# Kernel tuning notes

Measured on AMD Instinct MI355X. Metric: run time of the kernel, lower is better.

## Reference

```python
import jax, jax.numpy as jnp
import numpy as np

VOCAB = 32000
EMBED = 128
HIDDEN = 2048
LAYERS = 3
BATCH = 16


def setup_inputs() -> dict:
    key = jax.random.key(0)
    ks = jax.random.split(key, 4 + 4 * LAYERS)
    inp = {}
    inp["tokens"] = jax.random.randint(ks[0], (1, BATCH), 0, VOCAB, dtype=jnp.int64)
    inp["hidden"] = jax.random.normal(ks[1], (LAYERS, BATCH, HIDDEN), dtype=jnp.float32)
    s_e = 1.0 / np.sqrt(EMBED)
    s_h = 1.0 / np.sqrt(HIDDEN)
    inp["emb"] = jax.random.normal(ks[2], (VOCAB, EMBED), dtype=jnp.float32) * s_e
    for l in range(LAYERS):
        in_dim = EMBED if l == 0 else HIDDEN
        k0, k1, k2, k3 = jax.random.split(ks[4 + l], 4)
        inp[f"W_ih{l}"] = jax.random.normal(k0, (3 * HIDDEN, in_dim), dtype=jnp.float32) * s_h
        inp[f"W_hh{l}"] = jax.random.normal(k1, (3 * HIDDEN, HIDDEN), dtype=jnp.float32) * s_h
        inp[f"b_ih{l}"] = jax.random.normal(k2, (3 * HIDDEN,), dtype=jnp.float32) * s_h
        inp[f"b_hh{l}"] = jax.random.normal(k3, (3 * HIDDEN,), dtype=jnp.float32) * s_h
    inp["W_out"] = jax.random.normal(ks[3], (VOCAB, HIDDEN), dtype=jnp.float32) * s_h
    inp["b_out"] = jnp.zeros((VOCAB,), dtype=jnp.float32)
    return inp


def _gru_cell(x, h, W_ih, W_hh, b_ih, b_hh):
    # PyTorch GRU gate math; x: (B, in), h: (B, H)
    gi = x @ W_ih.T + b_ih  # (B, 3H)
    gh = h @ W_hh.T + b_hh  # (B, 3H)
    i_r, i_z, i_n = jnp.split(gi, 3, axis=-1)
    h_r, h_z, h_n = jnp.split(gh, 3, axis=-1)
    r = jax.nn.sigmoid(i_r + h_r)
    z = jax.nn.sigmoid(i_z + h_z)
    n = jnp.tanh(i_n + r * h_n)
    return (1.0 - z) * n + z * h


def reference(tokens, hidden, emb,
              W_ih0, W_hh0, b_ih0, b_hh0,
              W_ih1, W_hh1, b_ih1, b_hh1,
              W_ih2, W_hh2, b_ih2, b_hh2,
              W_out, b_out):
    # embedding + ReLU; tokens: (1, B) -> x: (B, E) (seq_len = 1)
    x = jax.nn.relu(emb[tokens[0]])
    Ws = [(W_ih0, W_hh0, b_ih0, b_hh0),
          (W_ih1, W_hh1, b_ih1, b_hh1),
          (W_ih2, W_hh2, b_ih2, b_hh2)]
    new_h = []
    inp = x
    for l, (Wih, Whh, bih, bhh) in enumerate(Ws):
        h_l = _gru_cell(inp, hidden[l], Wih, Whh, bih, bhh)
        new_h.append(h_l)
        inp = h_l  # top-layer output feeds next layer
    new_hidden = jnp.stack(new_h, axis=0)  # (L, B, H)
    logits = inp @ W_out.T + b_out  # (B, V)
    logp = jax.nn.log_softmax(logits, axis=1)
    return logp, new_hidden
```

## Files before the change

kernel.cpp:

```cpp
#include <hip/hip_runtime.h>
#include <cmath>


#define BB 16
#define HH 2048
#define EE 128
#define VV 32000
#define G3H (3 * HH)

__device__ __forceinline__ void fma4(float& a, const float4 w, const float4 x) {
  a = fmaf(w.x, x.x, a); a = fmaf(w.y, x.y, a);
  a = fmaf(w.z, x.z, a); a = fmaf(w.w, x.w, a);
}

__device__ __forceinline__ void glds16(const float* g, float* l) {
  __builtin_amdgcn_global_load_lds(
      (__attribute__((address_space(1))) void*)(g),
      (__attribute__((address_space(3))) void*)(l), 16, 0, 0);
}

__device__ __forceinline__ float foldpair(float a, float b, int m, int lane) {
  float t = (lane & m) ? a : b;
  t = __shfl_xor(t, m, 64);
  return ((lane & m) ? b : a) + t;
}

__device__ __forceinline__ float sel16(const float a[16], int i) {
  float s0 = (i & 1) ? a[1]  : a[0];
  float s1 = (i & 1) ? a[3]  : a[2];
  float s2 = (i & 1) ? a[5]  : a[4];
  float s3 = (i & 1) ? a[7]  : a[6];
  float s4 = (i & 1) ? a[9]  : a[8];
  float s5 = (i & 1) ? a[11] : a[10];
  float s6 = (i & 1) ? a[13] : a[12];
  float s7 = (i & 1) ? a[15] : a[14];
  float t0 = (i & 2) ? s1 : s0;
  float t1 = (i & 2) ? s3 : s2;
  float t2 = (i & 2) ? s5 : s4;
  float t3 = (i & 2) ? s7 : s6;
  float u0 = (i & 4) ? t1 : t0;
  float u1 = (i & 4) ? t3 : t2;
  return (i & 8) ? u1 : u0;
}

__device__ __forceinline__
void gemv_stream(const float* __restrict__ x,
                 const float* __restrict__ W,
                 float* __restrict__ planes,
                 int R, int slice, int row0, int nrows,
                 int lane, float* lds)
{
  const int ko = slice * 256 + lane * 4;
  float4 xv[16];
  #pragma unroll
  for (int b = 0; b < 16; ++b)
    xv[b] = *(const float4*)(x + b * HH + ko);

  const int idx = ((lane & 1) << 4) | ((lane & 2) << 2) | (lane & 4)
                | ((lane & 8) >> 2) | ((lane & 16) >> 4);
  const int rr = idx >> 4;
  const int bb = idx & 15;

  for (int m = 0; m < nrows; m += 8) {
    #pragma unroll
    for (int r = 0; r < 8; ++r)
      glds16(W + (size_t)(row0 + m + r) * HH + ko, lds + r * 256);
    asm volatile("s_waitcnt vmcnt(0)" ::: "memory");
    __builtin_amdgcn_sched_barrier(0);

    #pragma unroll
    for (int g = 0; g < 4; ++g) {
      float acc[32];
      #pragma unroll
      for (int i = 0; i < 32; ++i) acc[i] = 0.f;
      const float4 w0 = *(const float4*)(lds + (g * 2 + 0) * 256 + lane * 4);
      const float4 w1 = *(const float4*)(lds + (g * 2 + 1) * 256 + lane * 4);
      #pragma unroll
      for (int b = 0; b < 16; ++b) {
        fma4(acc[b],      w0, xv[b]);
        fma4(acc[16 + b], w1, xv[b]);
      }
      #pragma unroll
      for (int j = 0; j < 16; ++j) acc[j] = foldpair(acc[j], acc[j + 16], 1, lane);
      #pragma unroll
      for (int j = 0; j < 8; ++j)  acc[j] = foldpair(acc[j], acc[j + 8], 2, lane);
      #pragma unroll
      for (int j = 0; j < 4; ++j)  acc[j] = foldpair(acc[j], acc[j + 4], 4, lane);
      #pragma unroll
      for (int j = 0; j < 2; ++j)  acc[j] = foldpair(acc[j], acc[j + 2], 8, lane);
      acc[0] = foldpair(acc[0], acc[1], 16, lane);
      acc[0] += __shfl_xor(acc[0], 32, 64);
      if (lane < 32)
        planes[(size_t)(slice * 16 + bb) * R + row0 + m + g * 2 + rr] = acc[0];
    }
  }
}

__global__ __launch_bounds__(256, 3)
void gru_l0(const float* __restrict__ emb, const int* __restrict__ tokens,
            const float* __restrict__ hprev,
            const float* __restrict__ Wih0, const float* __restrict__ Whh0,
            float* __restrict__ gi_flat, float* __restrict__ ghP)
{
  __shared__ float lds[4 * 2048];
  const int tid  = threadIdx.x;
  const int lane = tid & 63;
  const int wv   = tid >> 6;
  const int bx   = blockIdx.x;

  if (bx < 128) {
    const int kk = lane & 15;
    const int rg = lane >> 4;
    const int u  = bx * 4 + wv;
    const int row0 = u * 12 + rg * 3;
    float acc[3][16];
    #pragma unroll
    for (int r = 0; r < 3; ++r)
      #pragma unroll
      for (int b = 0; b < 16; ++b) acc[r][b] = 0.f;

    #pragma unroll
    for (int it = 0; it < 2; ++it) {
      const int k = it * 64 + kk * 4;
      const float4 w0 = *(const float4*)(Wih0 + (size_t)row0 * EE + k);
      const float4 w1 = *(const float4*)(Wih0 + (size_t)(row0 + 1) * EE + k);
      const float4 w2 = *(const float4*)(Wih0 + (size_t)(row0 + 2) * EE + k);
      #pragma unroll
      for (int b = 0; b < 16; ++b) {
        float4 xv = *(const float4*)(emb + (size_t)tokens[b] * EE + k);
        xv.x = fmaxf(xv.x, 0.f); xv.y = fmaxf(xv.y, 0.f);
        xv.z = fmaxf(xv.z, 0.f); xv.w = fmaxf(xv.w, 0.f);
        fma4(acc[0][b], w0, xv);
        fma4(acc[1][b], w1, xv);
        fma4(acc[2][b], w2, xv);
      }
    }
    #pragma unroll
    for (int r = 0; r < 3; ++r) {
      #pragma unroll
      for (int b = 0; b < 16; ++b) {
        float a = acc[r][b];
        a += __shfl_xor(a, 1, 64);
        a += __shfl_xor(a, 2, 64);
        a += __shfl_xor(a, 4, 64);
        a += __shfl_xor(a, 8, 64);
        acc[r][b] = a;
      }
    }
    #pragma unroll
    for (int r = 0; r < 3; ++r)
      gi_flat[(size_t)kk * G3H + row0 + r] = sel16(acc[r], kk);
  } else {
    const int w = (bx - 128) * 4 + wv;
    gemv_stream(hprev, Whh0, ghP, G3H, w >> 7, (w & 127) * 48, 48,
                lane, lds + wv * 2048);
  }
}

__global__ __launch_bounds__(256, 3)
void gru_l12(const float* __restrict__ xprev, const float* __restrict__ hl,
             const float* __restrict__ Wih, const float* __restrict__ Whh,
             float* __restrict__ giP, float* __restrict__ ghP)
{
  __shared__ float lds[4 * 2048];
  const int lane = threadIdx.x & 63;
  const int wv   = threadIdx.x >> 6;
  const int bx   = blockIdx.x;
  if (bx < 256) {
    const int w = bx * 4 + wv;
    gemv_stream(xprev, Wih, giP, G3H, w >> 7, (w & 127) * 48, 48,
                lane, lds + wv * 2048);
  } else {
    const int w = (bx - 256) * 4 + wv;
    gemv_stream(hl, Whh, ghP, G3H, w >> 7, (w & 127) * 48, 48,
                lane, lds + wv * 2048);
  }
}

template<bool GI8>
__global__ __launch_bounds__(256)
void gru_epi(const float* __restrict__ gi_flat, const float* __restrict__ giP,
             const float* __restrict__ ghP,
             const float* __restrict__ bih, const float* __restrict__ bhh,
             const float* __restrict__ hprev, float* __restrict__ hout)
{
  const int idx = blockIdx.x * 256 + threadIdx.x;
  const int j = idx & (HH - 1);
  const int b = idx >> 11;
  float ir, iz, in_;
  if (GI8) {
    ir = 0.f; iz = 0.f; in_ = 0.f;
    #pragma unroll
    for (int s = 0; s < 8; ++s) {
      const size_t base = (size_t)(s * 16 + b) * G3H;
      ir  += giP[base + j];
      iz  += giP[base + HH + j];
      in_ += giP[base + 2 * HH + j];
    }
  } else {
    const size_t base = (size_t)b * G3H;
    ir  = gi_flat[base + j];
    iz  = gi_flat[base + HH + j];
    in_ = gi_flat[base + 2 * HH + j];
  }
  float hr = 0.f, hz = 0.f, hn = 0.f;
  #pragma unroll
  for (int s = 0; s < 8; ++s) {
    const size_t base = (size_t)(s * 16 + b) * G3H;
    hr += ghP[base + j];
    hz += ghP[base + HH + j];
    hn += ghP[base + 2 * HH + j];
  }
  ir += bih[j]; iz += bih[HH + j]; in_ += bih[2 * HH + j];
  hr += bhh[j]; hz += bhh[HH + j]; hn += bhh[2 * HH + j];
  const float r = 1.f / (1.f + expf(-(ir + hr)));
  const float z = 1.f / (1.f + expf(-(iz + hz)));
  const float n = tanhf(in_ + r * hn);
  hout[idx] = (1.f - z) * n + z * hprev[idx];
}

__global__ __launch_bounds__(256, 3)
void out_kernel(const float* __restrict__ h2, const float* __restrict__ Wout,
                float* __restrict__ opP)
{
  __shared__ float lds[4 * 2048];
  const int lane = threadIdx.x & 63;
  const int wv   = threadIdx.x >> 6;
  const int w = blockIdx.x * 4 + wv;
  const int slice = w / 250;
  const int part  = w % 250;
  gemv_stream(h2, Wout, opP, VV, slice, part * 128, 128, lane, lds + wv * 2048);
}

__global__ __launch_bounds__(1024)
void lsm_kernel(const float* __restrict__ opP, const float* __restrict__ bout,
                float* __restrict__ logp)
{
  const int b   = blockIdx.x;
  const int tid = threadIdx.x;
  float* row = logp + (size_t)b * VV;
  __shared__ float red[16];
  const int wv = tid >> 6, ln = tid & 63;

  float m = -3.4e38f;
  for (int i = tid; i < VV / 4; i += 1024) {
    float4 a = ((const float4*)bout)[i];
    #pragma unroll
    for (int s = 0; s < 8; ++s) {
      const float4 p = ((const float4*)(opP + (size_t)(s * 16 + b) * VV))[i];
      a.x += p.x; a.y += p.y; a.z += p.z; a.w += p.w;
    }
    ((float4*)row)[i] = a;
    m = fmaxf(m, fmaxf(fmaxf(a.x, a.y), fmaxf(a.z, a.w)));
  }
  #pragma unroll
  for (int s = 1; s < 64; s <<= 1) m = fmaxf(m, __shfl_xor(m, s, 64));
  if (ln == 0) red[wv] = m;
  __syncthreads();
  if (tid == 0) {
    float mm = red[0];
    for (int w = 1; w < 16; ++w) mm = fmaxf(mm, red[w]);
    red[0] = mm;
  }
  __syncthreads();
  const float M = red[0];
  __syncthreads();

  float s = 0.f;
  for (int i = tid; i < VV / 4; i += 1024) {
    float4 v = ((const float4*)row)[i];
    s += expf(v.x - M) + expf(v.y - M) + expf(v.z - M) + expf(v.w - M);
  }
  #pragma unroll
  for (int t = 1; t < 64; t <<= 1) s += __shfl_xor(s, t, 64);
  if (ln == 0) red[wv] = s;
  __syncthreads();
  if (tid == 0) {
    float ss = 0.f;
    for (int w = 0; w < 16; ++w) ss += red[w];
    red[0] = M + logf(ss);
  }
  __syncthreads();
  const float L = red[0];

  for (int i = tid; i < VV / 4; i += 1024) {
    float4 v = ((const float4*)row)[i];
    v.x -= L; v.y -= L; v.z -= L; v.w -= L;
    ((float4*)row)[i] = v;
  }
}

extern "C" void kernel_launch(void* const* d_in, const int* in_sizes, int n_in,
                              void* d_out, int out_size, void* d_ws, size_t ws_size,
                              hipStream_t stream)
{
  const int*   tokens = (const int*)d_in[0];
  const float* hidden = (const float*)d_in[1];
  const float* emb    = (const float*)d_in[2];
  const float* Wih0 = (const float*)d_in[3];
  const float* Whh0 = (const float*)d_in[4];
  const float* bih0 = (const float*)d_in[5];
  const float* bhh0 = (const float*)d_in[6];
  const float* Wih1 = (const float*)d_in[7];
  const float* Whh1 = (const float*)d_in[8];
  const float* bih1 = (const float*)d_in[9];
  const float* bhh1 = (const float*)d_in[10];
  const float* Wih2 = (const float*)d_in[11];
  const float* Whh2 = (const float*)d_in[12];
  const float* bih2 = (const float*)d_in[13];
  const float* bhh2 = (const float*)d_in[14];
  const float* Wout = (const float*)d_in[15];
  const float* bout = (const float*)d_in[16];

  float* outp = (float*)d_out;
  float* logp = outp;
  float* hnew = outp + (size_t)BB * VV;
  float* h0 = hnew;
  float* h1 = hnew + BB * HH;
  float* h2 = hnew + 2 * BB * HH;

  float* gi_flat = (float*)d_ws;
  float* giP = gi_flat + (size_t)BB * G3H;
  float* ghP = giP + (size_t)8 * BB * G3H;
  float* opP = ghP + (size_t)8 * BB * G3H;

  gru_l0<<<384, 256, 0, stream>>>(emb, tokens, hidden, Wih0, Whh0, gi_flat, ghP);
  gru_epi<false><<<128, 256, 0, stream>>>(gi_flat, nullptr, ghP, bih0, bhh0, hidden, h0);
  gru_l12<<<512, 256, 0, stream>>>(h0, hidden + BB * HH, Wih1, Whh1, giP, ghP);
  gru_epi<true><<<128, 256, 0, stream>>>(nullptr, giP, ghP, bih1, bhh1, hidden + BB * HH, h1);
  gru_l12<<<512, 256, 0, stream>>>(h1, hidden + 2 * BB * HH, Wih2, Whh2, giP, ghP);
  gru_epi<true><<<128, 256, 0, stream>>>(nullptr, giP, ghP, bih2, bhh2, hidden + 2 * BB * HH, h2);
  out_kernel<<<500, 256, 0, stream>>>(h2, Wout, opP);
  lsm_kernel<<<16, 1024, 0, stream>>>(opP, bout, logp);
}
```

Measured before the change: 231.2 us.

## Double-buffer weight streaming into LDS in GEMV kernels

```diff
diff --git a/kernel.cpp b/kernel.cpp
--- a/kernel.cpp
+++ b/kernel.cpp
@@ -44,10 +44,18 @@
 }
 
 __device__ __forceinline__
+void issue8(const float* __restrict__ W, int row0, int ko, float* buf) {
+  #pragma unroll
+  for (int r = 0; r < 8; ++r)
+    glds16(W + (size_t)(row0 + r) * HH + ko, buf + r * 256);
+}
+
+template<int NU>
+__device__ __forceinline__
 void gemv_stream(const float* __restrict__ x,
                  const float* __restrict__ W,
                  float* __restrict__ planes,
-                 int R, int slice, int row0, int nrows,
+                 int R, int slice, int row0,
                  int lane, float* lds)
 {
   const int ko = slice * 256 + lane * 4;
@@ -55,17 +63,24 @@
   #pragma unroll
   for (int b = 0; b < 16; ++b)
     xv[b] = *(const float4*)(x + b * HH + ko);
+  asm volatile("s_waitcnt vmcnt(0)" ::: "memory");
 
   const int idx = ((lane & 1) << 4) | ((lane & 2) << 2) | (lane & 4)
                 | ((lane & 8) >> 2) | ((lane & 16) >> 4);
   const int rr = idx >> 4;
   const int bb = idx & 15;
 
-  for (int m = 0; m < nrows; m += 8) {
-    #pragma unroll
-    for (int r = 0; r < 8; ++r)
-      glds16(W + (size_t)(row0 + m + r) * HH + ko, lds + r * 256);
-    asm volatile("s_waitcnt vmcnt(0)" ::: "memory");
+  issue8(W, row0, ko, lds);
+
+  for (int m = 0; m < NU; ++m) {
+    float* cur = (m & 1) ? lds + 2048 : lds;
+    float* nxt = (m & 1) ? lds : lds + 2048;
+    if (m + 1 < NU) {
+      issue8(W, row0 + (m + 1) * 8, ko, nxt);
+      asm volatile("s_waitcnt vmcnt(8)" ::: "memory");
+    } else {
+      asm volatile("s_waitcnt vmcnt(0)" ::: "memory");
+    }
     __builtin_amdgcn_sched_barrier(0);
 
     #pragma unroll
@@ -73,8 +88,8 @@
       float acc[32];
       #pragma unroll
       for (int i = 0; i < 32; ++i) acc[i] = 0.f;
-      const float4 w0 = *(const float4*)(lds + (g * 2 + 0) * 256 + lane * 4);
-      const float4 w1 = *(const float4*)(lds + (g * 2 + 1) * 256 + lane * 4);
+      const float4 w0 = *(const float4*)(cur + (g * 2 + 0) * 256 + lane * 4);
+      const float4 w1 = *(const float4*)(cur + (g * 2 + 1) * 256 + lane * 4);
       #pragma unroll
       for (int b = 0; b < 16; ++b) {
         fma4(acc[b],      w0, xv[b]);
@@ -91,18 +106,18 @@
       acc[0] = foldpair(acc[0], acc[1], 16, lane);
       acc[0] += __shfl_xor(acc[0], 32, 64);
       if (lane < 32)
-        planes[(size_t)(slice * 16 + bb) * R + row0 + m + g * 2 + rr] = acc[0];
-    }
-  }
-}
-
-__global__ __launch_bounds__(256, 3)
+        planes[(size_t)(slice * 16 + bb) * R + row0 + m * 8 + g * 2 + rr] = acc[0];
+    }
+  }
+}
+
+__global__ __launch_bounds__(256, 2)
 void gru_l0(const float* __restrict__ emb, const int* __restrict__ tokens,
             const float* __restrict__ hprev,
             const float* __restrict__ Wih0, const float* __restrict__ Whh0,
             float* __restrict__ gi_flat, float* __restrict__ ghP)
 {
-  __shared__ float lds[4 * 2048];
+  __shared__ float lds[4 * 4096];
   const int tid  = threadIdx.x;
   const int lane = tid & 63;
   const int wv   = tid >> 6;
@@ -152,28 +167,28 @@
       gi_flat[(size_t)kk * G3H + row0 + r] = sel16(acc[r], kk);
   } else {
     const int w = (bx - 128) * 4 + wv;
-    gemv_stream(hprev, Whh0, ghP, G3H, w >> 7, (w & 127) * 48, 48,
-                lane, lds + wv * 2048);
-  }
-}
-
-__global__ __launch_bounds__(256, 3)
+    gemv_stream<6>(hprev, Whh0, ghP, G3H, w >> 7, (w & 127) * 48,
+                   lane, lds + wv * 4096);
+  }
+}
+
+__global__ __launch_bounds__(256, 2)
 void gru_l12(const float* __restrict__ xprev, const float* __restrict__ hl,
              const float* __restrict__ Wih, const float* __restrict__ Whh,
              float* __restrict__ giP, float* __restrict__ ghP)
 {
-  __shared__ float lds[4 * 2048];
+  __shared__ float lds[4 * 4096];
   const int lane = threadIdx.x & 63;
   const int wv   = threadIdx.x >> 6;
   const int bx   = blockIdx.x;
   if (bx < 256) {
     const int w = bx * 4 + wv;
-    gemv_stream(xprev, Wih, giP, G3H, w >> 7, (w & 127) * 48, 48,
-                lane, lds + wv * 2048);
+    gemv_stream<6>(xprev, Wih, giP, G3H, w >> 7, (w & 127) * 48,
+                   lane, lds + wv * 4096);
   } else {
     const int w = (bx - 256) * 4 + wv;
-    gemv_stream(hl, Whh, ghP, G3H, w >> 7, (w & 127) * 48, 48,
-                lane, lds + wv * 2048);
+    gemv_stream<6>(hl, Whh, ghP, G3H, w >> 7, (w & 127) * 48,
+                   lane, lds + wv * 4096);
   }
 }
 
@@ -219,17 +234,17 @@
   hout[idx] = (1.f - z) * n + z * hprev[idx];
 }
 
-__global__ __launch_bounds__(256, 3)
+__global__ __launch_bounds__(256, 2)
 void out_kernel(const float* __restrict__ h2, const float* __restrict__ Wout,
                 float* __restrict__ opP)
 {
-  __shared__ float lds[4 * 2048];
+  __shared__ float lds[4 * 4096];
   const int lane = threadIdx.x & 63;
   const int wv   = threadIdx.x >> 6;
   const int w = blockIdx.x * 4 + wv;
   const int slice = w / 250;
   const int part  = w % 250;
-  gemv_stream(h2, Wout, opP, VV, slice, part * 128, 128, lane, lds + wv * 2048);
+  gemv_stream<16>(h2, Wout, opP, VV, slice, part * 128, lane, lds + wv * 4096);
 }
 
 __global__ __launch_bounds__(1024)
```

Result: faster. 225.2 us (-2.6%).
